# Kernel optimization log

Hardware: AMD Instinct MI355X
Metric: run time of the kernel (lower is better)

## Reference

```python
import jax, jax.numpy as jnp
import numpy as np

B, L, D, N_LAYERS = 128, 256, 512, 6
NEG = -9e15  # -9000000000000000.0 in the torch source


def _pair_coef(a1, L, D):
    # Faithful reduction of the torch repeat_interleave(dim=2) construction:
    # first half of a_input satisfies a_input[b, i, j, m] = h[b, i, (j*D + m)//L],
    # so sum_m a_input[...,m]*a1[m] = h[b,i] . c[j] with
    # c[j, f] = sum_{m : (j*D+m)//L == f} a1[m].
    j = jnp.arange(L)[:, None]
    m = jnp.arange(D)[None, :]
    idx = (j * D + m) // L  # [L, D], values in [0, D-1]
    c = jnp.zeros((L, D), a1.dtype)
    c = c.at[jnp.arange(L)[:, None], idx].add(jnp.broadcast_to(a1[None, :], (L, D)))
    return c


def gat_layer(x, adj, W, a):
    # h = x @ W; e[b,i,j] = relu(a_input[b,i,j,:] @ a)  (relu overwrites leakyrelu in source)
    h = x @ W  # [B, L, D]
    d = W.shape[1]
    a1, a2 = a[:d, 0], a[d:, 0]
    c = _pair_coef(a1, h.shape[1], d)  # [L, D]
    e = jax.nn.relu(jnp.einsum('bif,jf->bij', h, c) + (h @ a2)[:, None, :])
    att = jnp.where(adj > 0, e, NEG)
    att = jax.nn.softmax(att, axis=2)  # dropout is identity in eval
    h_prime = jnp.einsum('bij,bjd->bid', att, h)
    return jax.nn.elu(h_prime)  # concat=True branch


def position_weight(x, left_len, aspect_len, text_len):
    j = jnp.arange(x.shape[1])[None, :].astype(jnp.float32)  # [1, L]
    l = left_len[:, None].astype(jnp.float32)
    r = (left_len + aspect_len - 1)[:, None].astype(jnp.float32)
    tl = text_len[:, None].astype(jnp.float32)
    ctx = (text_len - aspect_len)[:, None].astype(jnp.float32)
    w = jnp.where(j < l, 1.0 - (l - j) / ctx,
        jnp.where(j <= r, 0.0,
        jnp.where(j < tl, 1.0 - (j - r) / ctx, 0.0)))
    return w[..., None].astype(x.dtype) * x


def aspect_mask(x, left_len, aspect_len):
    j = jnp.arange(x.shape[1])[None, :]
    l = left_len[:, None]
    r = (left_len + aspect_len - 1)[:, None]
    m = ((j >= l) & (j <= r)).astype(x.dtype)
    return m[..., None] * x


def setup_inputs() -> dict:
    key = jax.random.key(0)
    ks = jax.random.split(key, 6)
    x = jax.random.normal(ks[0], (B, L, D), jnp.float32)
    adj = jax.random.randint(ks[1], (B, L, L), 0, 2, jnp.int32)
    adj = adj.at[:, jnp.arange(L), jnp.arange(L)].set(1)  # self loops
    left_len = jax.random.randint(ks[2], (B,), 0, 20, jnp.int32)
    aspect_len = jax.random.randint(ks[3], (B,), 1, 6, jnp.int32)
    text_len = jnp.full((B,), L, jnp.int32)
    W_stack = jax.random.normal(ks[4], (N_LAYERS, D, D), jnp.float32) * (1.414 / np.sqrt(D))
    a_stack = jax.random.normal(ks[5], (N_LAYERS, 2 * D, 1), jnp.float32) * 0.05
    return {"x": x, "W_stack": W_stack, "a_stack": a_stack, "adj": adj,
            "left_len": left_len, "aspect_len": aspect_len, "text_len": text_len}


def reference(x, W_stack, a_stack, adj, left_len, aspect_len, text_len):
    text_out = x
    xp = position_weight(text_out, left_len, aspect_len, text_len)
    h1 = jax.nn.relu(gat_layer(xp, adj, W_stack[0], a_stack[0]))
    h1 = position_weight(h1, left_len, aspect_len, text_len)
    x_graph = jnp.zeros_like(h1)
    for i in range(1, N_LAYERS):
        x_graph = x_graph + jax.nn.relu(gat_layer(h1, adj, W_stack[i], a_stack[i]))
    x_graph = 0.2 * x_graph
    graph_mask = aspect_mask(x_graph, left_len, aspect_len)
    # hop == 1 attention pooling
    alpha_mat = jnp.einsum('bld,bmd->blm', graph_mask, text_out)  # [B, L, L]
    alpha = jax.nn.softmax(alpha_mat.sum(axis=1, keepdims=True), axis=2)  # [B, 1, L]
    a1 = jnp.einsum('blm,bmd->bld', alpha, text_out)[:, 0, :]  # [B, D]
    return a1
```

## Files before the change

kernel.cpp:

```cpp
#include <hip/hip_runtime.h>

#define NB 128
#define NLQ 256
#define ND 512
#define NLAYERS 6
#define DD (ND*ND)
#define MN (1024*ND)
#define HTB 131072

typedef _Float16 f16x8 __attribute__((ext_vector_type(8)));
typedef __fp16 fp16x2 __attribute__((ext_vector_type(2)));
typedef _Float16 f16x4v __attribute__((ext_vector_type(4)));
typedef float f32x4 __attribute__((ext_vector_type(4)));
typedef unsigned int u32x2 __attribute__((ext_vector_type(2)));
typedef unsigned int u32x4 __attribute__((ext_vector_type(4)));
typedef unsigned short ushort_t;

#define GLOAD16(gp, lp) __builtin_amdgcn_global_load_lds( \
    (const __attribute__((address_space(1))) void*)(gp), \
    (__attribute__((address_space(3))) void*)(lp), 16, 0, 0)

__device__ __forceinline__ float wave_max(float v){
  #pragma unroll
  for(int off=32; off; off>>=1) v = fmaxf(v, __shfl_xor(v, off));
  return v;
}
__device__ __forceinline__ float wave_sum(float v){
  #pragma unroll
  for(int off=32; off; off>>=1) v += __shfl_xor(v, off);
  return v;
}
__device__ __forceinline__ unsigned int pk16(float a, float b){
  fp16x2 h = __builtin_amdgcn_cvt_pkrtz(a, b);
  return __builtin_bit_cast(unsigned int, h);
}

__global__ __launch_bounds__(256) void k_scal(const float* __restrict__ a_stack,
                                              float* __restrict__ scal){
  int layer = blockIdx.x;
  const float* a = a_stack + (size_t)layer*2*ND;
  int t = threadIdx.x;
  float v0 = a[t];
  float v1 = a[256 + t];
  v0 = wave_sum(v0); v1 = wave_sum(v1);
  __shared__ float s0[4], s1[4];
  int wave = t>>6, lane = t&63;
  if(lane==0){ s0[wave]=v0; s1[wave]=v1; }
  __syncthreads();
  if(t==0){
    scal[layer*2+0] = s0[0]+s0[1]+s0[2]+s0[3];
    scal[layer*2+1] = s1[0]+s1[1]+s1[2]+s1[3];
  }
}

__global__ __launch_bounds__(256) void k_wa2(const float* __restrict__ Wst,
                                             const float* __restrict__ ast,
                                             float* __restrict__ v){
  int l  = blockIdx.x >> 7;
  int rg = blockIdx.x & 127;
  int i  = rg*4 + (threadIdx.x>>6);
  int lane = threadIdx.x & 63;
  const float4* wr = (const float4*)(Wst + (size_t)(l+1)*DD + (size_t)i*ND);
  const float4* ar = (const float4*)(ast + (size_t)(l+1)*2*ND + ND);
  float4 w0=wr[lane], w1=wr[lane+64], a0=ar[lane], a1=ar[lane+64];
  float d = w0.x*a0.x + w0.y*a0.y + w0.z*a0.z + w0.w*a0.w
          + w1.x*a1.x + w1.y*a1.y + w1.z*a1.z + w1.w*a1.w;
  d = wave_sum(d);
  if(lane==0) v[l*ND + i] = d;
}

__global__ __launch_bounds__(256) void k_wcvt(const float* __restrict__ Wsrc,
                                              ushort_t* __restrict__ Ho){
  __shared__ float CT[64][65];
  int bid = blockIdx.x;
  int l  = bid >> 6;
  int kt = (bid >> 3) & 7, nt = bid & 7;
  const float* Wl = Wsrc + (size_t)l*DD;
  int t = threadIdx.x;
  int r = t >> 2, c4 = (t&3)*16;
  #pragma unroll
  for(int u=0;u<4;u++){
    float4 vv = *(const float4*)(Wl + (size_t)(kt*64+r)*ND + nt*64 + c4 + u*4);
    CT[r][c4+u*4+0]=vv.x; CT[r][c4+u*4+1]=vv.y;
    CT[r][c4+u*4+2]=vv.z; CT[r][c4+u*4+3]=vv.w;
  }
  __syncthreads();
  int n = t >> 2, kc = t & 3;
  unsigned int o[8];
  #pragma unroll
  for(int j=0;j<8;j++)
    o[j] = pk16(CT[kc*16 + 2*j][n], CT[kc*16 + 2*j + 1][n]);
  ushort_t* dh = Ho + (size_t)l*DD + (size_t)(nt*64+n)*ND + kt*64 + kc*16;
  *(u32x4*)(dh)     = (u32x4){o[0],o[1],o[2],o[3]};
  *(u32x4*)(dh + 8) = (u32x4){o[4],o[5],o[6],o[7]};
}

__global__ __launch_bounds__(256) void k_xposw(const float* __restrict__ x,
    ushort_t* __restrict__ xp,
    const int* __restrict__ left, const int* __restrict__ asp, const int* __restrict__ tl){
  int c = blockIdx.x*256 + threadIdx.x;
  int row = c >> 6;
  int b = row >> 8;
  float jf = (float)(row & 255);
  float lf=(float)left[b], aspf=(float)asp[b], tlf=(float)tl[b];
  float rr=lf+aspf-1.f, ctx=tlf-aspf;
  float w;
  if(jf < lf)       w = 1.f-(lf-jf)/ctx;
  else if(jf <= rr) w = 0.f;
  else if(jf < tlf) w = 1.f-(jf-rr)/ctx;
  else              w = 0.f;
  const float4* xr = (const float4*)x;
  float4 v0 = xr[(size_t)c*2], v1 = xr[(size_t)c*2+1];
  u32x4 o = (u32x4){ pk16(v0.x*w, v0.y*w), pk16(v0.z*w, v0.w*w),
                     pk16(v1.x*w, v1.y*w), pk16(v1.z*w, v1.w*w) };
  *(u32x4*)(xp + (size_t)c*8) = o;
}

#define BKB 128
template<int MODE>
__device__ __forceinline__ void gemm_tile(const ushort_t* __restrict__ A16,
                                          const ushort_t* __restrict__ Wth,
                                          float* __restrict__ C,
                                          unsigned int* __restrict__ hP,
                                          ushort_t* __restrict__ Pbuf,
                                          float* __restrict__ tp4,
                                          const float* __restrict__ a2,
                                          const float* __restrict__ scal,
                                          int mtile, int ntile, unsigned char* lds){
  int t = threadIdx.x;
  int m0 = mtile*128, n0 = ntile*128;
  int lane = t & 63, wid = t >> 6;
  int wr = wid >> 2, wcq = wid & 3;
  int lrow = lane & 15, kb = lane >> 4;

  f32x4 acc[4][2];
  #pragma unroll
  for(int mi=0;mi<4;mi++)
    #pragma unroll
    for(int ni=0;ni<2;ni++)
      acc[mi][ni] = (f32x4){0.f,0.f,0.f,0.f};

  int s_row = t >> 3;
  int s_sl  = (t & 7) ^ (s_row & 7);
  int dstoff = wid*1024;

  const ushort_t* Asrc0 = A16 + (size_t)(m0 + s_row)*ND + s_sl*8;
  const ushort_t* Asrc1 = A16 + (size_t)(m0 + 64 + s_row)*ND + s_sl*8;
  const ushort_t* Bsrc0 = Wth + (size_t)(n0 + s_row)*ND + s_sl*8;
  const ushort_t* Bsrc1 = Wth + (size_t)(n0 + 64 + s_row)*ND + s_sl*8;

  GLOAD16(Asrc0, lds + dstoff);
  GLOAD16(Asrc1, lds + 8192 + dstoff);
  GLOAD16(Bsrc0, lds + 16384 + dstoff);
  GLOAD16(Bsrc1, lds + 24576 + dstoff);
  __syncthreads();

  int cur = 0;
  for(int it=0; it<8; ++it){
    if(it < 7){
      int kn = (it+1)*64;
      unsigned char* dst = lds + ((cur^1)<<15);
      GLOAD16(Asrc0 + kn, dst + dstoff);
      GLOAD16(Asrc1 + kn, dst + 8192 + dstoff);
      GLOAD16(Bsrc0 + kn, dst + 16384 + dstoff);
      GLOAD16(Bsrc1 + kn, dst + 24576 + dstoff);
    }
    unsigned char* Ab = lds + (cur<<15);
    unsigned char* Bb = Ab + 16384;
    #pragma unroll
    for(int ks=0; ks<2; ks++){
      f16x8 ah[4], bh[2];
      #pragma unroll
      for(int mi=0;mi<4;mi++){
        int ar = wr*64 + mi*16 + lrow;
        int sl = (ks*4 + kb) ^ (ar & 7);
        ah[mi] = *(const f16x8*)(Ab + ar*BKB + sl*16);
      }
      #pragma unroll
      for(int ni=0;ni<2;ni++){
        int br = wcq*32 + ni*16 + lrow;
        int sl = (ks*4 + kb) ^ (br & 7);
        bh[ni] = *(const f16x8*)(Bb + br*BKB + sl*16);
      }
      #pragma unroll
      for(int mi=0;mi<4;mi++)
        #pragma unroll
        for(int ni=0;ni<2;ni++)
          acc[mi][ni] = __builtin_amdgcn_mfma_f32_16x16x32_f16(ah[mi], bh[ni], acc[mi][ni], 0,0,0);
    }
    __syncthreads();
    cur ^= 1;
  }

  int rg = lane >> 4;
  int cc = lane & 15;
  if(MODE == 0){
    #pragma unroll
    for(int mi=0;mi<4;mi++)
      #pragma unroll
      for(int ni=0;ni<2;ni++){
        int col = n0 + wcq*32 + ni*16 + cc;
        #pragma unroll
        for(int q=0;q<4;q++){
          int row = m0 + wr*64 + mi*16 + rg*4 + q;
          C[(size_t)row*ND + col] = acc[mi][ni][q];
        }
      }
  } else {
    float S0 = scal[0], S1 = scal[1];
    float* CT = (float*)lds;
    int b = m0 >> 8;
    int ibase = m0 & 255;
    int tr   = t >> 2;
    int tch  = t & 3;
    float tpsum = 0.f;
    #pragma unroll
    for(int p=0;p<2;p++){
      if((wcq>>1) == p){
        #pragma unroll
        for(int mi=0;mi<4;mi++)
          #pragma unroll
          for(int ni=0;ni<2;ni++)
            #pragma unroll
            for(int q=0;q<4;q++)
              CT[((wcq&1)*32 + ni*16 + cc)*130 + wr*64 + mi*16 + rg*4 + q] = acc[mi][ni][q];
      }
      __syncthreads();
      int lcol = t >> 6;
      int lrow2 = (t & 63)*2;
      #pragma unroll
      for(int u=0;u<8;u++){
        int c = lcol + u*8;
        float2 v2 = *(float2*)&CT[c*130 + lrow2];
        size_t uidx = ((size_t)b*HTB + (size_t)(n0 + p*64 + c)*256 + ibase + lrow2) >> 1;
        hP[uidx] = pk16(v2.x, v2.y);
      }
      {
        int cpr = t & 31;
        int rq  = t >> 5;
        #pragma unroll
        for(int rr2=0; rr2<8; rr2++){
          int row = rq*8 + rr2;
          float pval = S0*CT[(2*cpr)*130 + row] + S1*CT[(2*cpr+1)*130 + row];
          int ig = ibase + row;
          _Float16 ph = (_Float16)pval;
          size_t addr = (size_t)b*262144 + (size_t)(ig>>5)*32768
                      + (size_t)(ig&31)*256 + (n0>>1) + p*32 + cpr;
          Pbuf[addr] = __builtin_bit_cast(unsigned short, ph);
        }
      }
      #pragma unroll
      for(int cc2=0; cc2<16; cc2++){
        int c = tch*16 + cc2;
        tpsum = fmaf(CT[c*130 + tr], a2[n0 + p*64 + c], tpsum);
      }
      __syncthreads();
    }
    tpsum += __shfl_xor(tpsum, 1);
    tpsum += __shfl_xor(tpsum, 2);
    if(tch == 0) tp4[(n0>>7)*32768 + m0 + tr] = tpsum;
  }
}

__global__ __launch_bounds__(512) void k_gemm_t(const ushort_t* __restrict__ A16,
                                                const ushort_t* __restrict__ Wth,
                                                unsigned int* __restrict__ hP,
                                                ushort_t* __restrict__ Pbuf,
                                                float* __restrict__ tp4,
                                                const float* __restrict__ a2,
                                                const float* __restrict__ scal){
  __shared__ unsigned char lds[65536];
  int bid = blockIdx.x;
  int ntile = (bid >> 3) & 3;
  int mtile = (bid & 7) | ((bid >> 5) << 3);
  gemm_tile<1>(A16, Wth, nullptr, hP, Pbuf, tp4, a2, scal, mtile, ntile, lds);
}

__global__ __launch_bounds__(512) void k_gemm_b(const ushort_t* __restrict__ Abase, long aStride,
                                                const ushort_t* __restrict__ Wth,
                                                float* __restrict__ Cbase){
  __shared__ unsigned char lds[65536];
  int l  = blockIdx.x >> 5;
  int tb = blockIdx.x & 31;
  gemm_tile<0>(Abase + (size_t)l*aStride, Wth + (size_t)l*DD,
               Cbase + (size_t)l*MN, nullptr, nullptr, nullptr,
               nullptr, nullptr, tb>>2, tb&3, lds);
}

__global__ __launch_bounds__(256) void k_attn0(
    const ushort_t* __restrict__ hTH,
    const int* __restrict__ adj,
    const float* __restrict__ tpart,
    const int* __restrict__ left, const int* __restrict__ asp, const int* __restrict__ tl,
    float* __restrict__ PA){
  __shared__ unsigned char attH[32*512];
  __shared__ unsigned char BsH[16384];

  int bid = blockIdx.x;
  int b  = bid & 127;
  int ic = bid >> 7;
  int i0 = ic*32;
  int tid = threadIdx.x;
  int lane = tid & 63, w = tid >> 6;
  const ushort_t* HH = hTH + (size_t)b*HTB;
  const ushort_t* Pt = (const ushort_t*)PA + (size_t)b*262144 + (size_t)ic*32768;

  float t0v=0.f, t1v=0.f, t2v=0.f, t3v=0.f;
  #pragma unroll
  for(int nt=0; nt<4; nt++){
    float4 tv = ((const float4*)(tpart + nt*32768 + b*256))[lane];
    t0v += tv.x; t1v += tv.y; t2v += tv.z; t3v += tv.w;
  }

  for(int rr=0; rr<8; rr++){
    int il = w*8 + rr;
    int i  = i0 + il;
    f16x4v pv = *(const f16x4v*)(Pt + il*256 + lane*4);
    int4 av = ((const int4*)(adj + ((size_t)b*NLQ + i)*NLQ))[lane];
    float e0 = fmaxf((float)pv[0] + t0v, 0.f);
    float e1 = fmaxf((float)pv[1] + t1v, 0.f);
    float e2 = fmaxf((float)pv[2] + t2v, 0.f);
    float e3 = fmaxf((float)pv[3] + t3v, 0.f);
    float m = -3.0e38f;
    if(av.x>0) m = e0;
    if(av.y>0) m = fmaxf(m, e1);
    if(av.z>0) m = fmaxf(m, e2);
    if(av.w>0) m = fmaxf(m, e3);
    m = wave_max(m);
    float p0 = (av.x>0) ? __expf(e0-m) : 0.f;
    float p1 = (av.y>0) ? __expf(e1-m) : 0.f;
    float p2 = (av.z>0) ? __expf(e2-m) : 0.f;
    float p3 = (av.w>0) ? __expf(e3-m) : 0.f;
    float s = wave_sum(p0+p1+p2+p3);
    float inv = 1.f/s;
    unsigned int w0 = pk16(p0*inv, p1*inv);
    unsigned int w1 = pk16(p2*inv, p3*inv);
    int off = il*512 + ((lane*8) ^ ((il&7)<<4));
    *(u32x2*)(attH + off) = (u32x2){w0,w1};
  }

  int wm = w >> 1, wn = w & 1;
  int lrow = lane & 15, kb = lane >> 4;
  int rg = lane >> 4, cc = lane & 15;
  float lf=(float)left[b], aspf=(float)asp[b], tlf=(float)tl[b];
  float rrv=lf+aspf-1.f, ctx=tlf-aspf;
  int arow = wm*16 + lrow;
  int aswz = (arow&7)<<4;

  for(int dp=0; dp<2; dp++){
    int d0 = dp*256;
    f32x4 acc[8];
    #pragma unroll
    for(int ni=0;ni<8;ni++) acc[ni] = (f32x4){0.f,0.f,0.f,0.f};
    for(int ks=0; ks<8; ks++){
      int j0 = ks*32;
      __syncthreads();
      #pragma unroll
      for(int u=0;u<4;u++){
        int chunk = (u*4 + w)*64 + lane;
        int row = chunk >> 2, sl = chunk & 3;
        GLOAD16(HH + (size_t)(d0+row)*256 + j0 + sl*8, BsH + (u*4+w)*1024);
      }
      __syncthreads();
      int aoff = arow*512 + ((j0*2 + kb*16) ^ aswz);
      f16x8 ah = *(const f16x8*)(attH + aoff);
      #pragma unroll
      for(int ni=0; ni<8; ni++){
        f16x8 bh = *(const f16x8*)(BsH + (wn*128 + ni*16 + lrow)*64 + kb*16);
        acc[ni] = __builtin_amdgcn_mfma_f32_16x16x32_f16(ah, bh, acc[ni], 0,0,0);
      }
    }
    #pragma unroll
    for(int q=0;q<4;q++){
      int row = i0 + wm*16 + rg*4 + q;
      float fi = (float)row;
      float wgt;
      if(fi < lf)        wgt = 1.f-(lf-fi)/ctx;
      else if(fi <= rrv) wgt = 0.f;
      else if(fi < tlf)  wgt = 1.f-(fi-rrv)/ctx;
      else               wgt = 0.f;
      #pragma unroll
      for(int ni=0;ni<8;ni++){
        int col = d0 + wn*128 + ni*16 + cc;
        PA[((size_t)b*NLQ + row)*ND + col] = wgt*fmaxf(acc[ni][q], 0.f);
      }
    }
  }
}

__global__ __launch_bounds__(256) void k_tv(const float* __restrict__ h1,
                                            const float* __restrict__ v,
                                            float* __restrict__ T){
  int row  = blockIdx.x*4 + (threadIdx.x>>6);
  int lane = threadIdx.x & 63;
  const float4* hr = (const float4*)(h1 + (size_t)row*ND);
  float4 h0 = hr[lane], h1v = hr[lane+64];
  float s0,s1,s2,s3,s4;
  #define DOTV(SL, L) { \
    const float4* vr = (const float4*)(v + (L)*ND); \
    float4 v0 = vr[lane], v1 = vr[lane+64]; \
    float dd = h0.x*v0.x+h0.y*v0.y+h0.z*v0.z+h0.w*v0.w \
             + h1v.x*v1.x+h1v.y*v1.y+h1v.z*v1.z+h1v.w*v1.w; \
    SL = wave_sum(dd); }
  DOTV(s0,0) DOTV(s1,1) DOTV(s2,2) DOTV(s3,3) DOTV(s4,4)
  #undef DOTV
  if(lane==0){
    T[0*32768 + row]=s0; T[1*32768 + row]=s1; T[2*32768 + row]=s2;
    T[3*32768 + row]=s3; T[4*32768 + row]=s4;
  }
}

__global__ __launch_bounds__(256) void k_rows(const float* __restrict__ h1,
                                              const int* __restrict__ left, const int* __restrict__ asp,
                                              ushort_t* __restrict__ R){
  int b = blockIdx.x;
  int nk = asp[b], l0 = left[b];
  const float* src = h1 + (size_t)b*NLQ*ND;
  unsigned int* dst = (unsigned int*)(R + (size_t)b*8*ND);
  #pragma unroll
  for(int u=0; u<8; u++){
    int idx = threadIdx.x + u*256;
    int k = idx >> 8, c = idx & 255;
    float2 vv = (k<nk) ? ((const float2*)(src + (size_t)(l0+k)*ND))[c] : (float2){0.f,0.f};
    dst[idx] = pk16(vv.x, vv.y);
  }
}

__global__ __launch_bounds__(256) void k_att5(const float* __restrict__ h1,
    const float* __restrict__ Hasp, const float* __restrict__ T,
    const int* __restrict__ adj, const float* __restrict__ scal,
    const int* __restrict__ left, const int* __restrict__ asp,
    ushort_t* __restrict__ y){
  __shared__ float att[5][260];
  int b  = blockIdx.x & 127;
  int l  = blockIdx.x >> 7;
  int tid = threadIdx.x, lane = tid&63, w = tid>>6;
  int nk = asp[b], l0 = left[b];
  float S0 = scal[2*(l+1)], S1 = scal[2*(l+1)+1];

  for(int k = w; k < 5; k += 4){
    if(k < nk){
      const float2* hrow = (const float2*)(Hasp + (size_t)l*MN + (size_t)(b*8+k)*ND);
      const int* arow = adj + ((size_t)b*NLQ + (l0+k))*NLQ;
      const float* Tl = T + l*32768 + b*256;
      float e[4]; int av[4];
      float m = -3.0e38f;
      #pragma unroll
      for(int q=0;q<4;q++){
        int j = lane + 64*q;
        float2 hp = hrow[j];
        av[q] = arow[j];
        e[q] = fmaxf(S0*hp.x + S1*hp.y + Tl[j], 0.f);
        if(av[q] > 0) m = fmaxf(m, e[q]);
      }
      m = wave_max(m);
      float pp[4]; float s = 0.f;
      #pragma unroll
      for(int q=0;q<4;q++){
        pp[q] = (av[q] > 0) ? __expf(e[q]-m) : 0.f;
        s += pp[q];
      }
      s = wave_sum(s);
      float inv = 1.f/s;
      #pragma unroll
      for(int q=0;q<4;q++) att[k][lane+64*q] = pp[q]*inv;
    } else {
      #pragma unroll
      for(int q=0;q<4;q++) att[k][lane+64*q] = 0.f;
    }
  }
  __syncthreads();

  int d = tid;
  const float* hb = h1 + (size_t)b*NLQ*ND;
  float ax[5] = {0,0,0,0,0}, ay[5] = {0,0,0,0,0};
  for(int jj=0; jj<NLQ; jj++){
    float hx = hb[(size_t)jj*ND + d];
    float hy = hb[(size_t)jj*ND + 256 + d];
    #pragma unroll
    for(int k=0;k<5;k++){
      float a = att[k][jj];
      ax[k] += a*hx;
      ay[k] += a*hy;
    }
  }
  ushort_t* yb = y + (size_t)l*MN + (size_t)b*8*ND;
  #pragma unroll
  for(int k=0;k<5;k++){
    yb[(size_t)k*ND + d]       = __builtin_bit_cast(unsigned short, (_Float16)ax[k]);
    yb[(size_t)k*ND + 256 + d] = __builtin_bit_cast(unsigned short, (_Float16)ay[k]);
  }
  #pragma unroll
  for(int u=0;u<6;u++) yb[5*ND + u*256 + tid] = 0;
}

__global__ __launch_bounds__(256) void k_g(const float* __restrict__ hp,
    const int* __restrict__ asp, float* __restrict__ g){
  int b = blockIdx.x, d = threadIdx.x;
  int nk = asp[b];
  float gx=0.f, gy=0.f;
  for(int l=0;l<5;l++){
    for(int k=0;k<nk;k++){
      const float* r = hp + (size_t)l*MN + (size_t)(b*8+k)*ND;
      gx += fmaxf(r[d], 0.f);
      gy += fmaxf(r[d+256], 0.f);
    }
  }
  g[b*ND + d]       = 0.2f*gx;
  g[b*ND + 256 + d] = 0.2f*gy;
}

__global__ __launch_bounds__(256) void k_dot(const float* __restrict__ x,
    const float* __restrict__ g, float* __restrict__ s){
  int row  = blockIdx.x*4 + (threadIdx.x>>6);
  int b    = row >> 8;
  int lane = threadIdx.x & 63;
  const float4* xr = (const float4*)(x + (size_t)row*ND);
  const float4* gr = (const float4*)(g + (size_t)b*ND);
  float4 x0=xr[lane], x1=xr[lane+64], g0=gr[lane], g1=gr[lane+64];
  float d = x0.x*g0.x + x0.y*g0.y + x0.z*g0.z + x0.w*g0.w
          + x1.x*g1.x + x1.y*g1.y + x1.z*g1.z + x1.w*g1.w;
  d = wave_sum(d);
  if(lane==0) s[row] = d;
}

__global__ __launch_bounds__(256) void k_out(const float* __restrict__ x,
    const float* __restrict__ s, float* __restrict__ out){
  int b  = blockIdx.x >> 2;
  int ch = blockIdx.x & 3;
  int tid = threadIdx.x, lane = tid&63, w = tid>>6;
  __shared__ float red[4];
  __shared__ float alpha[NLQ];
  __shared__ float part[128];
  float sv = s[b*NLQ + tid];
  float m = wave_max(sv);
  if(lane==0) red[w] = m;
  __syncthreads();
  m = fmaxf(fmaxf(red[0],red[1]), fmaxf(red[2],red[3]));
  float p = __expf(sv - m);
  float su = wave_sum(p);
  __syncthreads();
  if(lane==0) red[w] = su;
  __syncthreads();
  su = red[0]+red[1]+red[2]+red[3];
  alpha[tid] = p/su;
  __syncthreads();
  int d = ch*128 + (tid & 127);
  int half = tid >> 7;
  const float* xb = x + (size_t)b*NLQ*ND;
  float acc = 0.f;
  for(int mm = half*128; mm < half*128 + 128; mm++)
    acc += alpha[mm] * xb[(size_t)mm*ND + d];
  if(half) part[tid & 127] = acc;
  __syncthreads();
  if(!half) out[(size_t)b*ND + d] = acc + part[tid & 127];
}

extern "C" void kernel_launch(void* const* d_in, const int* in_sizes, int n_in,
                              void* d_out, int out_size, void* d_ws, size_t ws_size,
                              hipStream_t stream){
  const float* x    = (const float*)d_in[0];
  const float* Wst  = (const float*)d_in[1];
  const float* ast  = (const float*)d_in[2];
  const int*   adj  = (const int*)d_in[3];
  const int*   left = (const int*)d_in[4];
  const int*   asp  = (const int*)d_in[5];
  const int*   tl   = (const int*)d_in[6];
  float* out = (float*)d_out;
  float* ws  = (float*)d_ws;

  const size_t SZ = (size_t)NB*NLQ*ND;
  float* bufA = ws;
  float* bufB = ws + SZ;
  float* ws2  = ws + 2*SZ;
  float* tpart= ws2;
  float* T    = tpart + 4*32768;
  float* g    = T + 163840;
  float* scal = g + 65536;
  float* v    = scal + 16;
  float* sbuf = v + 2560;
  ushort_t* w0th = (ushort_t*)(sbuf + 32768);

  ushort_t* hTH  = (ushort_t*)bufB;
  ushort_t* xp16 = (ushort_t*)(bufB + (SZ>>1));

  float* Hasp = bufB;
  ushort_t* y16 = (ushort_t*)(Hasp + (size_t)5*MN);
  float* hp   = Hasp + (size_t)10*MN;
  ushort_t* R16 = (ushort_t*)(hp + (size_t)5*MN);
  ushort_t* wt15h = (ushort_t*)(hp + (size_t)5*MN + (MN>>1));

  k_scal<<<NLAYERS, 256, 0, stream>>>(ast, scal);
  k_wa2<<<5*128, 256, 0, stream>>>(Wst, ast, v);
  k_wcvt<<<64, 256, 0, stream>>>(Wst, w0th);
  k_xposw<<<8192, 256, 0, stream>>>(x, xp16, left, asp, tl);

  k_gemm_t<<<(NB*NLQ/128)*(ND/128), 512, 0, stream>>>(xp16, w0th,
      (unsigned int*)hTH, (ushort_t*)bufA, tpart, ast + ND, scal);
  k_attn0<<<NB*8, 256, 0, stream>>>(hTH, adj, tpart, left, asp, tl, bufA);

  k_wcvt<<<5*64, 256, 0, stream>>>(Wst + DD, wt15h);
  k_tv<<<NB*NLQ/4, 256, 0, stream>>>(bufA, v, T);
  k_rows<<<NB, 256, 0, stream>>>(bufA, left, asp, R16);
  k_gemm_b<<<5*32, 512, 0, stream>>>(R16, 0L, wt15h, Hasp);
  k_att5<<<5*NB, 256, 0, stream>>>(bufA, Hasp, T, adj, scal, left, asp, y16);
  k_gemm_b<<<5*32, 512, 0, stream>>>(y16, (long)MN, wt15h, hp);
  k_g<<<NB, 256, 0, stream>>>(hp, asp, g);

  k_dot<<<NB*NLQ/4, 256, 0, stream>>>(x, g, sbuf);
  k_out<<<NB*4, 256, 0, stream>>>(x, sbuf, out);
}
```

Measured before the change: 218.8 us.

## Store activations and input in fp16, fold position weight into GEMM epilogue

Position weighting moves out of the input conversion kernel and into the first GEMM epilogue, where it is applied per row to the accumulator (valid because the weight is a per-row scale). The converted fp16 copy of x is then reused by k_dot and k_out in place of the fp32 input. The layer-1 output h1 is now written as fp16 rather than fp32, which roughly halves the traffic for k_tv, k_rows and k_att5. Buffer layout is reorganized (smaller Pbuf stride) to make room, at the cost of reduced precision in the final attention pooling and in the intermediate activations.

```diff
diff --git a/kernel.cpp b/kernel.cpp
--- a/kernel.cpp
+++ b/kernel.cpp
@@ -33,6 +33,9 @@
 __device__ __forceinline__ unsigned int pk16(float a, float b){
   fp16x2 h = __builtin_amdgcn_cvt_pkrtz(a, b);
   return __builtin_bit_cast(unsigned int, h);
+}
+__device__ __forceinline__ float f16u(ushort_t u){
+  return (float)__builtin_bit_cast(_Float16, u);
 }
 
 __global__ __launch_bounds__(256) void k_scal(const float* __restrict__ a_stack,
@@ -95,24 +98,13 @@
   *(u32x4*)(dh + 8) = (u32x4){o[4],o[5],o[6],o[7]};
 }
 
-__global__ __launch_bounds__(256) void k_xposw(const float* __restrict__ x,
-    ushort_t* __restrict__ xp,
-    const int* __restrict__ left, const int* __restrict__ asp, const int* __restrict__ tl){
+__global__ __launch_bounds__(256) void k_xcvt(const float* __restrict__ x,
+                                              ushort_t* __restrict__ xp){
   int c = blockIdx.x*256 + threadIdx.x;
-  int row = c >> 6;
-  int b = row >> 8;
-  float jf = (float)(row & 255);
-  float lf=(float)left[b], aspf=(float)asp[b], tlf=(float)tl[b];
-  float rr=lf+aspf-1.f, ctx=tlf-aspf;
-  float w;
-  if(jf < lf)       w = 1.f-(lf-jf)/ctx;
-  else if(jf <= rr) w = 0.f;
-  else if(jf < tlf) w = 1.f-(jf-rr)/ctx;
-  else              w = 0.f;
   const float4* xr = (const float4*)x;
   float4 v0 = xr[(size_t)c*2], v1 = xr[(size_t)c*2+1];
-  u32x4 o = (u32x4){ pk16(v0.x*w, v0.y*w), pk16(v0.z*w, v0.w*w),
-                     pk16(v1.x*w, v1.y*w), pk16(v1.z*w, v1.w*w) };
+  u32x4 o = (u32x4){ pk16(v0.x, v0.y), pk16(v0.z, v0.w),
+                     pk16(v1.x, v1.y), pk16(v1.z, v1.w) };
   *(u32x4*)(xp + (size_t)c*8) = o;
 }
 
@@ -126,6 +118,9 @@
                                           float* __restrict__ tp4,
                                           const float* __restrict__ a2,
                                           const float* __restrict__ scal,
+                                          const int* __restrict__ left,
+                                          const int* __restrict__ asp,
+                                          const int* __restrict__ tl,
                                           int mtile, int ntile, unsigned char* lds){
   int t = threadIdx.x;
   int m0 = mtile*128, n0 = ntile*128;
@@ -211,6 +206,23 @@
     float* CT = (float*)lds;
     int b = m0 >> 8;
     int ibase = m0 & 255;
+    {
+      float lf=(float)left[b], aspf=(float)asp[b], tlf=(float)tl[b];
+      float rrow=lf+aspf-1.f, inv_ctx=1.f/(tlf-aspf);
+      #pragma unroll
+      for(int mi=0;mi<4;mi++)
+        #pragma unroll
+        for(int q=0;q<4;q++){
+          float jf = (float)(ibase + wr*64 + mi*16 + rg*4 + q);
+          float w;
+          if(jf < lf)         w = 1.f-(lf-jf)*inv_ctx;
+          else if(jf <= rrow) w = 0.f;
+          else if(jf < tlf)   w = 1.f-(jf-rrow)*inv_ctx;
+          else                w = 0.f;
+          acc[mi][0][q] *= w;
+          acc[mi][1][q] *= w;
+        }
+    }
     int tr   = t >> 2;
     int tch  = t & 3;
     float tpsum = 0.f;
@@ -244,7 +256,7 @@
           float pval = S0*CT[(2*cpr)*130 + row] + S1*CT[(2*cpr+1)*130 + row];
           int ig = ibase + row;
           _Float16 ph = (_Float16)pval;
-          size_t addr = (size_t)b*262144 + (size_t)(ig>>5)*32768
+          size_t addr = (size_t)b*65536 + (size_t)(ig>>5)*8192
                       + (size_t)(ig&31)*256 + (n0>>1) + p*32 + cpr;
           Pbuf[addr] = __builtin_bit_cast(unsigned short, ph);
         }
@@ -268,12 +280,16 @@
                                                 ushort_t* __restrict__ Pbuf,
                                                 float* __restrict__ tp4,
                                                 const float* __restrict__ a2,
-                                                const float* __restrict__ scal){
+                                                const float* __restrict__ scal,
+                                                const int* __restrict__ left,
+                                                const int* __restrict__ asp,
+                                                const int* __restrict__ tl){
   __shared__ unsigned char lds[65536];
   int bid = blockIdx.x;
   int ntile = (bid >> 3) & 3;
   int mtile = (bid & 7) | ((bid >> 5) << 3);
-  gemm_tile<1>(A16, Wth, nullptr, hP, Pbuf, tp4, a2, scal, mtile, ntile, lds);
+  gemm_tile<1>(A16, Wth, nullptr, hP, Pbuf, tp4, a2, scal, left, asp, tl,
+               mtile, ntile, lds);
 }
 
 __global__ __launch_bounds__(512) void k_gemm_b(const ushort_t* __restrict__ Abase, long aStride,
@@ -284,15 +300,16 @@
   int tb = blockIdx.x & 31;
   gemm_tile<0>(Abase + (size_t)l*aStride, Wth + (size_t)l*DD,
                Cbase + (size_t)l*MN, nullptr, nullptr, nullptr,
-               nullptr, nullptr, tb>>2, tb&3, lds);
+               nullptr, nullptr, nullptr, nullptr, nullptr, tb>>2, tb&3, lds);
 }
 
 __global__ __launch_bounds__(256) void k_attn0(
     const ushort_t* __restrict__ hTH,
+    const ushort_t* __restrict__ Pbuf,
     const int* __restrict__ adj,
     const float* __restrict__ tpart,
     const int* __restrict__ left, const int* __restrict__ asp, const int* __restrict__ tl,
-    float* __restrict__ PA){
+    ushort_t* __restrict__ h16){
   __shared__ unsigned char attH[32*512];
   __shared__ unsigned char BsH[16384];
 
@@ -303,7 +320,7 @@
   int tid = threadIdx.x;
   int lane = tid & 63, w = tid >> 6;
   const ushort_t* HH = hTH + (size_t)b*HTB;
-  const ushort_t* Pt = (const ushort_t*)PA + (size_t)b*262144 + (size_t)ic*32768;
+  const ushort_t* Pt = Pbuf + (size_t)b*65536 + (size_t)ic*8192;
 
   float t0v=0.f, t1v=0.f, t2v=0.f, t3v=0.f;
   #pragma unroll
@@ -382,25 +399,29 @@
       #pragma unroll
       for(int ni=0;ni<8;ni++){
         int col = d0 + wn*128 + ni*16 + cc;
-        PA[((size_t)b*NLQ + row)*ND + col] = wgt*fmaxf(acc[ni][q], 0.f);
-      }
-    }
-  }
-}
-
-__global__ __launch_bounds__(256) void k_tv(const float* __restrict__ h1,
+        float ov = wgt*fmaxf(acc[ni][q], 0.f);
+        h16[((size_t)b*NLQ + row)*ND + col] =
+            __builtin_bit_cast(unsigned short, (_Float16)ov);
+      }
+    }
+  }
+}
+
+__global__ __launch_bounds__(256) void k_tv(const ushort_t* __restrict__ h16,
                                             const float* __restrict__ v,
                                             float* __restrict__ T){
   int row  = blockIdx.x*4 + (threadIdx.x>>6);
   int lane = threadIdx.x & 63;
-  const float4* hr = (const float4*)(h1 + (size_t)row*ND);
-  float4 h0 = hr[lane], h1v = hr[lane+64];
+  f16x8 hv = *(const f16x8*)(h16 + (size_t)row*ND + lane*8);
+  float hf[8];
+  #pragma unroll
+  for(int i=0;i<8;i++) hf[i] = (float)hv[i];
   float s0,s1,s2,s3,s4;
   #define DOTV(SL, L) { \
     const float4* vr = (const float4*)(v + (L)*ND); \
-    float4 v0 = vr[lane], v1 = vr[lane+64]; \
-    float dd = h0.x*v0.x+h0.y*v0.y+h0.z*v0.z+h0.w*v0.w \
-             + h1v.x*v1.x+h1v.y*v1.y+h1v.z*v1.z+h1v.w*v1.w; \
+    float4 v0 = vr[lane*2], v1 = vr[lane*2+1]; \
+    float dd = hf[0]*v0.x+hf[1]*v0.y+hf[2]*v0.z+hf[3]*v0.w \
+             + hf[4]*v1.x+hf[5]*v1.y+hf[6]*v1.z+hf[7]*v1.w; \
     SL = wave_sum(dd); }
   DOTV(s0,0) DOTV(s1,1) DOTV(s2,2) DOTV(s3,3) DOTV(s4,4)
   #undef DOTV
@@ -410,23 +431,22 @@
   }
 }
 
-__global__ __launch_bounds__(256) void k_rows(const float* __restrict__ h1,
+__global__ __launch_bounds__(256) void k_rows(const ushort_t* __restrict__ h16,
                                               const int* __restrict__ left, const int* __restrict__ asp,
                                               ushort_t* __restrict__ R){
   int b = blockIdx.x;
   int nk = asp[b], l0 = left[b];
-  const float* src = h1 + (size_t)b*NLQ*ND;
+  const unsigned int* src = (const unsigned int*)(h16 + (size_t)b*NLQ*ND);
   unsigned int* dst = (unsigned int*)(R + (size_t)b*8*ND);
   #pragma unroll
   for(int u=0; u<8; u++){
     int idx = threadIdx.x + u*256;
     int k = idx >> 8, c = idx & 255;
-    float2 vv = (k<nk) ? ((const float2*)(src + (size_t)(l0+k)*ND))[c] : (float2){0.f,0.f};
-    dst[idx] = pk16(vv.x, vv.y);
-  }
-}
-
-__global__ __launch_bounds__(256) void k_att5(const float* __restrict__ h1,
+    dst[idx] = (k<nk) ? src[(size_t)(l0+k)*256 + c] : 0u;
+  }
+}
+
+__global__ __launch_bounds__(256) void k_att5(const ushort_t* __restrict__ h16,
     const float* __restrict__ Hasp, const float* __restrict__ T,
     const int* __restrict__ adj, const float* __restrict__ scal,
     const int* __restrict__ left, const int* __restrict__ asp,
@@ -472,11 +492,11 @@
   __syncthreads();
 
   int d = tid;
-  const float* hb = h1 + (size_t)b*NLQ*ND;
+  const ushort_t* hb = h16 + (size_t)b*NLQ*ND;
   float ax[5] = {0,0,0,0,0}, ay[5] = {0,0,0,0,0};
   for(int jj=0; jj<NLQ; jj++){
-    float hx = hb[(size_t)jj*ND + d];
-    float hy = hb[(size_t)jj*ND + 256 + d];
+    float hx = f16u(hb[(size_t)jj*ND + d]);
+    float hy = f16u(hb[(size_t)jj*ND + 256 + d]);
     #pragma unroll
     for(int k=0;k<5;k++){
       float a = att[k][jj];
@@ -510,21 +530,21 @@
   g[b*ND + 256 + d] = 0.2f*gy;
 }
 
-__global__ __launch_bounds__(256) void k_dot(const float* __restrict__ x,
+__global__ __launch_bounds__(256) void k_dot(const ushort_t* __restrict__ x16,
     const float* __restrict__ g, float* __restrict__ s){
   int row  = blockIdx.x*4 + (threadIdx.x>>6);
   int b    = row >> 8;
   int lane = threadIdx.x & 63;
-  const float4* xr = (const float4*)(x + (size_t)row*ND);
+  f16x8 xv = *(const f16x8*)(x16 + (size_t)row*ND + lane*8);
   const float4* gr = (const float4*)(g + (size_t)b*ND);
-  float4 x0=xr[lane], x1=xr[lane+64], g0=gr[lane], g1=gr[lane+64];
-  float d = x0.x*g0.x + x0.y*g0.y + x0.z*g0.z + x0.w*g0.w
-          + x1.x*g1.x + x1.y*g1.y + x1.z*g1.z + x1.w*g1.w;
+  float4 g0 = gr[lane*2], g1 = gr[lane*2+1];
+  float d = (float)xv[0]*g0.x + (float)xv[1]*g0.y + (float)xv[2]*g0.z + (float)xv[3]*g0.w
+          + (float)xv[4]*g1.x + (float)xv[5]*g1.y + (float)xv[6]*g1.z + (float)xv[7]*g1.w;
   d = wave_sum(d);
   if(lane==0) s[row] = d;
 }
 
-__global__ __launch_bounds__(256) void k_out(const float* __restrict__ x,
+__global__ __launch_bounds__(256) void k_out(const ushort_t* __restrict__ x16,
     const float* __restrict__ s, float* __restrict__ out){
   int b  = blockIdx.x >> 2;
   int ch = blockIdx.x & 3;
@@ -547,10 +567,10 @@
   __syncthreads();
   int d = ch*128 + (tid & 127);
   int half = tid >> 7;
-  const float* xb = x + (size_t)b*NLQ*ND;
+  const ushort_t* xb = x16 + (size_t)b*NLQ*ND;
   float acc = 0.f;
   for(int mm = half*128; mm < half*128 + 128; mm++)
-    acc += alpha[mm] * xb[(size_t)mm*ND + d];
+    acc += alpha[mm] * f16u(xb[(size_t)mm*ND + d]);
   if(half) part[tid & 127] = acc;
   __syncthreads();
   if(!half) out[(size_t)b*ND + d] = acc + part[tid & 127];
@@ -581,32 +601,38 @@
   float* sbuf = v + 2560;
   ushort_t* w0th = (ushort_t*)(sbuf + 32768);
 
+  ushort_t* Pbuf = (ushort_t*)bufA;
+  ushort_t* h16  = Pbuf + (size_t)NB*65536;
+
   ushort_t* hTH  = (ushort_t*)bufB;
-  ushort_t* xp16 = (ushort_t*)(bufB + (SZ>>1));
+  ushort_t* x16  = (ushort_t*)(bufB + (SZ>>1));
 
   float* Hasp = bufB;
   ushort_t* y16 = (ushort_t*)(Hasp + (size_t)5*MN);
-  float* hp   = Hasp + (size_t)10*MN;
-  ushort_t* R16 = (ushort_t*)(hp + (size_t)5*MN);
-  ushort_t* wt15h = (ushort_t*)(hp + (size_t)5*MN + (MN>>1));
+  float* hp   = (float*)(y16 + (size_t)5*MN);
+  {
+  }
+  float* hpF  = bufB + (size_t)5*MN + (size_t)5*MN/2;
+  ushort_t* R16 = (ushort_t*)(hpF + (size_t)5*MN);
+  ushort_t* wt15h = (ushort_t*)((float*)R16 + (size_t)MN/2);
 
   k_scal<<<NLAYERS, 256, 0, stream>>>(ast, scal);
   k_wa2<<<5*128, 256, 0, stream>>>(Wst, ast, v);
   k_wcvt<<<64, 256, 0, stream>>>(Wst, w0th);
-  k_xposw<<<8192, 256, 0, stream>>>(x, xp16, left, asp, tl);
-
-  k_gemm_t<<<(NB*NLQ/128)*(ND/128), 512, 0, stream>>>(xp16, w0th,
-      (unsigned int*)hTH, (ushort_t*)bufA, tpart, ast + ND, scal);
-  k_attn0<<<NB*8, 256, 0, stream>>>(hTH, adj, tpart, left, asp, tl, bufA);
+  k_xcvt<<<8192, 256, 0, stream>>>(x, x16);
+
+  k_gemm_t<<<(NB*NLQ/128)*(ND/128), 512, 0, stream>>>(x16, w0th,
+      (unsigned int*)hTH, Pbuf, tpart, ast + ND, scal, left, asp, tl);
+  k_attn0<<<NB*8, 256, 0, stream>>>(hTH, Pbuf, adj, tpart, left, asp, tl, h16);
 
   k_wcvt<<<5*64, 256, 0, stream>>>(Wst + DD, wt15h);
-  k_tv<<<NB*NLQ/4, 256, 0, stream>>>(bufA, v, T);
-  k_rows<<<NB, 256, 0, stream>>>(bufA, left, asp, R16);
+  k_tv<<<NB*NLQ/4, 256, 0, stream>>>(h16, v, T);
+  k_rows<<<NB, 256, 0, stream>>>(h16, left, asp, R16);
   k_gemm_b<<<5*32, 512, 0, stream>>>(R16, 0L, wt15h, Hasp);
-  k_att5<<<5*NB, 256, 0, stream>>>(bufA, Hasp, T, adj, scal, left, asp, y16);
-  k_gemm_b<<<5*32, 512, 0, stream>>>(y16, (long)MN, wt15h, hp);
-  k_g<<<NB, 256, 0, stream>>>(hp, asp, g);
-
-  k_dot<<<NB*NLQ/4, 256, 0, stream>>>(x, g, sbuf);
-  k_out<<<NB*4, 256, 0, stream>>>(x, sbuf, out);
-}
+  k_att5<<<5*NB, 256, 0, stream>>>(h16, Hasp, T, adj, scal, left, asp, y16);
+  k_gemm_b<<<5*32, 512, 0, stream>>>(y16, (long)MN, wt15h, hpF);
+  k_g<<<NB, 256, 0, stream>>>(hpF, asp, g);
+
+  k_dot<<<NB*NLQ/4, 256, 0, stream>>>(x16, g, sbuf);
+  k_out<<<NB*4, 256, 0, stream>>>(x16, sbuf, out);
+}
```

Result: faster. 213.2 us (-2.6%).
